# Optimization experiments

Hardware: AMD Instinct MI355X
Metric: run time of the kernel (lower is better)

Reference implementation:

```python
import jax, jax.numpy as jnp
import numpy as np

TOP_K = 2

def setup_inputs() -> dict:
    key = jax.random.key(0)
    k1, k2, k3, k4 = jax.random.split(key, 4)
    N, H, F, E = 2048, 1024, 2048, 8
    x = jax.random.normal(k1, (N, H), dtype=jnp.float32)
    router_weight = jax.random.normal(k2, (H, E), dtype=jnp.float32) * 0.02
    w1 = jax.random.normal(k3, (E, H, F), dtype=jnp.float32) * 0.02
    w2 = jax.random.normal(k4, (E, F, H), dtype=jnp.float32) * 0.02
    return {"x": x, "router_weight": router_weight, "w1": w1, "w2": w2}

def reference(x, router_weight, w1, w2):
    # Router: softmax over experts, top-k, renormalize (matches torch forward).
    N = x.shape[0]
    E = router_weight.shape[1]
    logits = x.astype(jnp.float32) @ router_weight            # [N, E]
    rprobs = jax.nn.softmax(logits, axis=-1)
    topk_p, topk_i = jax.lax.top_k(rprobs, TOP_K)             # [N, K]
    topk_p = topk_p / jnp.sum(topk_p, axis=-1, keepdims=True)
    # Scatter normalized top-k probs into dense [N, E] gate matrix; zeros
    # everywhere else, so gating subsumes the boolean routing_map.
    probs = jnp.zeros((N, E), dtype=jnp.float32).at[
        jnp.arange(N)[:, None], topk_i].set(topk_p)
    # Expert FFN (same math as permute -> grouped GEMM -> weighted scatter-add:
    # out[t] = sum_e probs[t,e] * gelu(x[t] @ w1[e]) @ w2[e]).
    h = jnp.einsum('nh,ehf->enf', x, w1)                      # [E, N, F]
    h = jax.nn.gelu(h, approximate=False)                     # torch F.gelu is erf-based
    y = jnp.einsum('enf,efh->enh', h, w2)                     # [E, N, H]
    out = jnp.einsum('enh,ne->nh', y, probs.astype(x.dtype))  # weighted combine
    return out
```

## Files before the change

### kernel.cpp

```cpp
#include <hip/hip_runtime.h>
#include <hip/hip_fp16.h>
#include <math.h>

#define NTOK 2048
#define HID  1024
#define FFN  2048
#define NEXP 8

#define BM 128
#define BN 128
#define BK 32
#define LDK 36
#define MAX_TILES 40
#define TLDA 66

#define WS_COUNTS 0
#define WS_SEG    32
#define WS_PROBS  128
#define WS_LISTS  (128 + NTOK*NEXP*4)
#define WS_XH     262144
#define WS_W2T    (WS_XH + NTOK*HID*2)
#define WS_HBUF   (WS_W2T + (size_t)NEXP*HID*FFN*2)

typedef _Float16 half8 __attribute__((ext_vector_type(8)));
typedef __fp16   fp16x2 __attribute__((ext_vector_type(2)));
typedef float    f32x4 __attribute__((ext_vector_type(4)));
typedef unsigned long long u64;

static __device__ __forceinline__ unsigned short f2h_bits(float f) {
  union { _Float16 h; unsigned short u; } v;
  v.h = (_Float16)f;
  return v.u;
}
static __device__ __forceinline__ unsigned pack2(float a, float b) {
  union { fp16x2 h; unsigned u; } v;
  v.h[0] = (__fp16)a; v.h[1] = (__fp16)b;
  return v.u;
}
static __device__ __forceinline__ unsigned cvt2(float a, float b) {
  union { fp16x2 h; unsigned u; } t;
  t.h = __builtin_amdgcn_cvt_pkrtz(a, b);
  return t.u;
}

#define GLOAD16(gsrc, ldst) \
  __builtin_amdgcn_global_load_lds( \
      (const __attribute__((address_space(1))) unsigned int*)(gsrc), \
      (__attribute__((address_space(3))) unsigned int*)(ldst), 16, 0, 0)

#define VMCNT0 asm volatile("s_waitcnt vmcnt(0)" ::: "memory")

template<int IS_W1>
static __device__ __forceinline__ void transpose4(
    int t0, const float* __restrict__ wsrc, unsigned short* __restrict__ wdst,
    unsigned short (*Ls)[64*TLDA], int tid)
{
  const int row = tid >> 2, cq = tid & 3;
  const int oc  = tid >> 2, rs = tid & 3;
  const int e = t0 >> 9;
  const int R = IS_W1 ? HID : FFN;
  const int C = IS_W1 ? FFN : HID;
  const float* src = wsrc + (size_t)e * HID * FFN;
  unsigned short* dst = wdst + (size_t)e * HID * FFN;
  float4 ld[2][4];

#define TGEOM(tt, r0v, c0v) \
    { const int rem_ = (t0 + (tt)) & 511; \
      r0v = IS_W1 ? ((rem_ >> 5) * 64) : ((rem_ >> 4) * 64); \
      c0v = IS_W1 ? ((rem_ & 31) * 64) : ((rem_ & 15) * 64); }

  {
    int r0, c0; TGEOM(0, r0, c0);
    const float4* sp = reinterpret_cast<const float4*>(
        src + (size_t)(r0 + row) * C + c0 + cq * 16);
#pragma unroll
    for (int j = 0; j < 4; ++j) ld[0][j] = sp[j];
  }
#pragma unroll
  for (int t = 0; t < 4; ++t) {
    if (t < 3) {
      int r0, c0; TGEOM(t + 1, r0, c0);
      const float4* sp = reinterpret_cast<const float4*>(
          src + (size_t)(r0 + row) * C + c0 + cq * 16);
#pragma unroll
      for (int j = 0; j < 4; ++j) ld[(t + 1) & 1][j] = sp[j];
    }
    {
      unsigned* Ld = reinterpret_cast<unsigned*>(Ls[t & 1]);
      const int dbase = row * (TLDA / 2) + cq * 8;
      const float4 a = ld[t & 1][0], b = ld[t & 1][1];
      const float4 c2 = ld[t & 1][2], d = ld[t & 1][3];
      Ld[dbase + 0] = pack2(a.x, a.y);  Ld[dbase + 1] = pack2(a.z, a.w);
      Ld[dbase + 2] = pack2(b.x, b.y);  Ld[dbase + 3] = pack2(b.z, b.w);
      Ld[dbase + 4] = pack2(c2.x, c2.y); Ld[dbase + 5] = pack2(c2.z, c2.w);
      Ld[dbase + 6] = pack2(d.x, d.y);  Ld[dbase + 7] = pack2(d.z, d.w);
    }
    __syncthreads();
    {
      int r0, c0; TGEOM(t, r0, c0);
      unsigned v[8];
#pragma unroll
      for (int j = 0; j < 8; ++j) {
        unsigned lo = Ls[t & 1][(rs * 16 + 2 * j    ) * TLDA + oc];
        unsigned hi = Ls[t & 1][(rs * 16 + 2 * j + 1) * TLDA + oc];
        v[j] = lo | (hi << 16);
      }
      unsigned short* dp = dst + (size_t)(c0 + oc) * R + r0 + rs * 16;
      *reinterpret_cast<uint4*>(dp)     = (uint4){v[0], v[1], v[2], v[3]};
      *reinterpret_cast<uint4*>(dp + 8) = (uint4){v[4], v[5], v[6], v[7]};
    }
  }
#undef TGEOM
}

__global__ __launch_bounds__(256) void moe_prep(
    const float* __restrict__ x, const float* __restrict__ rw,
    unsigned short* __restrict__ xh,
    int* __restrict__ counts, int* __restrict__ lists, float* __restrict__ probs)
{
  const int tid = threadIdx.x;
  const int wid = tid >> 6, lane = tid & 63;
  const int t = blockIdx.x * 4 + wid;

  const float* xr = x + (size_t)t * HID + lane * 16;
  const float4* xp = reinterpret_cast<const float4*>(xr);
  float4 v0 = xp[0], v1 = xp[1], v2 = xp[2], v3 = xp[3];
  float xv[16] = {v0.x,v0.y,v0.z,v0.w, v1.x,v1.y,v1.z,v1.w,
                  v2.x,v2.y,v2.z,v2.w, v3.x,v3.y,v3.z,v3.w};
  float acc[NEXP];
#pragma unroll
  for (int e = 0; e < NEXP; ++e) acc[e] = 0.f;
#pragma unroll
  for (int j = 0; j < 16; ++j) {
    const float4* rp = reinterpret_cast<const float4*>(rw + (size_t)(lane*16 + j) * NEXP);
    float4 a = rp[0], b = rp[1];
    acc[0] += xv[j]*a.x; acc[1] += xv[j]*a.y; acc[2] += xv[j]*a.z; acc[3] += xv[j]*a.w;
    acc[4] += xv[j]*b.x; acc[5] += xv[j]*b.y; acc[6] += xv[j]*b.z; acc[7] += xv[j]*b.w;
  }
#pragma unroll
  for (int off = 32; off > 0; off >>= 1) {
#pragma unroll
    for (int e = 0; e < NEXP; ++e) acc[e] += __shfl_down(acc[e], off);
  }
  unsigned short* xd = xh + (size_t)t * HID + lane * 16;
  *reinterpret_cast<uint4*>(xd) =
      (uint4){pack2(v0.x,v0.y), pack2(v0.z,v0.w), pack2(v1.x,v1.y), pack2(v1.z,v1.w)};
  *reinterpret_cast<uint4*>(xd + 8) =
      (uint4){pack2(v2.x,v2.y), pack2(v2.z,v2.w), pack2(v3.x,v3.y), pack2(v3.z,v3.w)};
  if (lane == 0) {
    float m = acc[0];
#pragma unroll
    for (int e = 1; e < NEXP; ++e) m = fmaxf(m, acc[e]);
    float p[NEXP];
#pragma unroll
    for (int e = 0; e < NEXP; ++e) p[e] = expf(acc[e] - m);
    int i0 = 0;
#pragma unroll
    for (int e = 1; e < NEXP; ++e) if (p[e] > p[i0]) i0 = e;
    int i1 = -1;
#pragma unroll
    for (int e = 0; e < NEXP; ++e) {
      if (e == i0) continue;
      if (i1 < 0 || p[e] > p[i1]) i1 = e;
    }
    const float inv = 1.f / (p[i0] + p[i1]);
    probs[t * NEXP + i0] = p[i0] * inv;
    probs[t * NEXP + i1] = p[i1] * inv;
    int pos0 = atomicAdd(&counts[i0], 1); lists[i0 * NTOK + pos0] = t;
    int pos1 = atomicAdd(&counts[i1], 1); lists[i1 * NTOK + pos1] = t;
  }
}

__global__ void moe_segoff(const int* __restrict__ counts, int* __restrict__ seg) {
  if (threadIdx.x == 0 && blockIdx.x == 0) {
    int run = 0;
    for (int e = 0; e < NEXP; ++e) {
      seg[e] = run;
      run += ((counts[e] + BM - 1) / BM) * BM;
    }
    seg[NEXP] = run;
  }
}

__global__ __launch_bounds__(256) void moe_k2(
    const unsigned short* __restrict__ xh, const float* __restrict__ w1,
    const float* __restrict__ w2, unsigned short* __restrict__ w2t,
    const int* __restrict__ counts, const int* __restrict__ seg,
    const int* __restrict__ lists, unsigned short* __restrict__ hbuf)
{
  __shared__ __align__(16) unsigned short SMEM[2*BM*BK + 2*128*LDK];
  __shared__ int tokL[BM];
  const int bid = blockIdx.x;
  const int tid = threadIdx.x;

  if (bid >= MAX_TILES * 16) {
    transpose4<0>((bid - MAX_TILES * 16) * 4, w2, w2t,
                  reinterpret_cast<unsigned short(*)[64 * TLDA]>(SMEM), tid);
    return;
  }

  const int tile = bid >> 4;
  const int jcol = bid & 15;
  const int rb = tile * BM;
  if (rb >= seg[NEXP]) return;
  int e = 0;
#pragma unroll
  for (int q = 1; q < NEXP; ++q) if (seg[q] <= rb) e = q;
  const int cnt = counts[e];
  const int rloc0 = rb - seg[e];

  unsigned short (*Asm)[BM*BK]   = reinterpret_cast<unsigned short(*)[BM*BK]>(SMEM);
  unsigned short (*Bsm)[128*LDK] = reinterpret_cast<unsigned short(*)[128*LDK]>(SMEM + 2*BM*BK);

  if (tid < BM) {
    int rl = rloc0 + tid;
    tokL[tid] = (rl < cnt) ? lists[e * NTOK + rl] : 0;
  }
  __syncthreads();

  const int lane = tid & 63;
  const int wid = tid >> 6;
  const int wr = (wid >> 1) * 64;
  const int wc = (wid & 1) * 64;
  const int lr = (lane >> 4) * 4;
  const int lc = lane & 15;
  const int khi = (lane >> 4) * 8;

  const int cw8 = (lane & 3) * 8;
  const int r0 = wid*16 + (lane >> 2);
  const unsigned short* abase[2];
  abase[0] = xh + (size_t)tokL[r0]      * HID + cw8;
  abase[1] = xh + (size_t)tokL[64 + r0] * HID + cw8;

  const int kb = tid >> 5;
  const int fb = tid & 31;
  const float* bbase = w1 + (size_t)e * HID * FFN + (size_t)jcol * 128 + fb * 4;

  f32x4 acc[4][4];
#pragma unroll
  for (int m = 0; m < 4; ++m)
#pragma unroll
    for (int n = 0; n < 4; ++n)
      acc[m][n] = (f32x4){0.f, 0.f, 0.f, 0.f};

  f32x4 bld[4];

#define LOADB1(kk) do { \
    _Pragma("unroll") \
    for (int j = 0; j < 4; ++j) \
      bld[j] = *reinterpret_cast<const f32x4*>(bbase + (size_t)((kk) + kb*4 + j) * FFN); \
  } while (0)

#define STAGEA1(buf, kk) do { \
    GLOAD16(abase[0] + (kk), &Asm[buf][(wid*64)*8]); \
    GLOAD16(abase[1] + (kk), &Asm[buf][(256 + wid*64)*8]); \
  } while (0)

#define CVTB1(buf) do { \
    _Pragma("unroll") \
    for (int i3 = 0; i3 < 4; ++i3) { \
      uint2 wv; \
      wv.x = cvt2(bld[0][i3], bld[1][i3]); \
      wv.y = cvt2(bld[2][i3], bld[3][i3]); \
      *reinterpret_cast<uint2*>(&Bsm[buf][(fb*4 + i3)*LDK + kb*4]) = wv; \
    } } while (0)

  LOADB1(0);
  STAGEA1(0, 0);
  int cur = 0;
  for (int kk = 0; kk < HID; kk += BK) {
    CVTB1(cur);
    VMCNT0;
    __syncthreads();
    if (kk + BK < HID) {
      LOADB1(kk + BK);
      STAGEA1(cur ^ 1, kk + BK);
    }
    half8 af[4], bf[4];
#pragma unroll
    for (int m = 0; m < 4; ++m)
      af[m] = *reinterpret_cast<const half8*>(&Asm[cur][(wr + m*16 + lc)*BK + khi]);
#pragma unroll
    for (int n = 0; n < 4; ++n) {
      union { u64 q[2]; half8 h; } t;
      const unsigned short* bp = &Bsm[cur][(wc + n*16 + lc)*LDK + khi];
      t.q[0] = *reinterpret_cast<const u64*>(bp);
      t.q[1] = *reinterpret_cast<const u64*>(bp + 4);
      bf[n] = t.h;
    }
#pragma unroll
    for (int m = 0; m < 4; ++m)
#pragma unroll
      for (int n = 0; n < 4; ++n)
        acc[m][n] = __builtin_amdgcn_mfma_f32_16x16x32_f16(af[m], bf[n], acc[m][n], 0, 0, 0);
    cur ^= 1;
  }
#undef LOADB1
#undef STAGEA1
#undef CVTB1

#pragma unroll
  for (int m = 0; m < 4; ++m) {
#pragma unroll
    for (int r = 0; r < 4; ++r) {
      unsigned short* hp = hbuf + (size_t)(rb + wr + m*16 + lr + r) * FFN + jcol*128 + wc + lc;
#pragma unroll
      for (int n = 0; n < 4; ++n) {
        float v = acc[m][n][r];
        float g = 0.5f * v * (1.f + erff(v * 0.70710678118f));
        hp[n*16] = f2h_bits(g);
      }
    }
  }
}

__global__ __launch_bounds__(256) void moe_gemm2(
    const unsigned short* __restrict__ hbuf, const unsigned short* __restrict__ w2t,
    const int* __restrict__ counts, const int* __restrict__ seg,
    const int* __restrict__ lists, const float* __restrict__ probs,
    float* __restrict__ out)
{
  const int tile = blockIdx.x >> 4;
  const int jcol = (blockIdx.x >> 1) & 7;
  const int ks   = blockIdx.x & 1;
  const int rb = tile * BM;
  if (rb >= seg[NEXP]) return;
  int e = 0;
#pragma unroll
  for (int q = 1; q < NEXP; ++q) if (seg[q] <= rb) e = q;
  const int cnt = counts[e];
  const int rloc0 = rb - seg[e];
  const int k0 = ks * (FFN / 2);
  const int k1 = k0 + (FFN / 2);

  __shared__ int tokL[BM];
  __shared__ float pL[BM];
  __shared__ __align__(16) unsigned short Asm[2][BM*BK];
  __shared__ __align__(16) unsigned short Bsm[2][BM*BK];

  const int tid = threadIdx.x;
  if (tid < BM) {
    int rl = rloc0 + tid;
    if (rl < cnt) {
      int tk = lists[e * NTOK + rl];
      tokL[tid] = tk;
      pL[tid] = probs[tk * NEXP + e];
    } else { tokL[tid] = 0; pL[tid] = 0.f; }
  }
  __syncthreads();

  const int lane = tid & 63;
  const int wid = tid >> 6;
  const int wr = (wid >> 1) * 64;
  const int wc = (wid & 1) * 64;
  const int lr = (lane >> 4) * 4;
  const int lc = lane & 15;
  const int khi = (lane >> 4) * 8;

  const int cw8 = (lane & 3) * 8;
  const int r0 = wid*16 + (lane >> 2);
  const unsigned short* abase[2];
  const unsigned short* bbase[2];
  abase[0] = hbuf + (size_t)(rb + r0)      * FFN + cw8;
  abase[1] = hbuf + (size_t)(rb + 64 + r0) * FFN + cw8;
  bbase[0] = w2t + ((size_t)e * HID + jcol*BN + r0)      * FFN + cw8;
  bbase[1] = w2t + ((size_t)e * HID + jcol*BN + 64 + r0) * FFN + cw8;

  f32x4 acc[4][4];
#pragma unroll
  for (int m = 0; m < 4; ++m)
#pragma unroll
    for (int n = 0; n < 4; ++n)
      acc[m][n] = (f32x4){0.f, 0.f, 0.f, 0.f};

#define STAGE2(buf, kk) do { \
    _Pragma("unroll") \
    for (int i = 0; i < 2; ++i) { \
      GLOAD16(abase[i] + (kk), &Asm[buf][(i*256 + wid*64)*8]); \
      GLOAD16(bbase[i] + (kk), &Bsm[buf][(i*256 + wid*64)*8]); \
    } } while (0)

  STAGE2(0, k0);
  VMCNT0;
  __syncthreads();
  int cur = 0;
  for (int kk = k0; kk < k1; kk += BK) {
    if (kk + BK < k1) STAGE2(cur ^ 1, kk + BK);
    half8 af[4], bf[4];
#pragma unroll
    for (int m = 0; m < 4; ++m)
      af[m] = *reinterpret_cast<const half8*>(&Asm[cur][(wr + m*16 + lc)*BK + khi]);
#pragma unroll
    for (int n = 0; n < 4; ++n)
      bf[n] = *reinterpret_cast<const half8*>(&Bsm[cur][(wc + n*16 + lc)*BK + khi]);
#pragma unroll
    for (int m = 0; m < 4; ++m)
#pragma unroll
      for (int n = 0; n < 4; ++n)
        acc[m][n] = __builtin_amdgcn_mfma_f32_16x16x32_f16(af[m], bf[n], acc[m][n], 0, 0, 0);
    VMCNT0;
    __syncthreads();
    cur ^= 1;
  }
#undef STAGE2

#pragma unroll
  for (int m = 0; m < 4; ++m) {
#pragma unroll
    for (int r = 0; r < 4; ++r) {
      const int lrow = wr + m*16 + lr + r;
      const int rl = rloc0 + lrow;
      if (rl >= cnt) continue;
      const int tok = tokL[lrow];
      const float p = pL[lrow];
      float* op = out + (size_t)tok * HID + jcol*BN + wc + lc;
#pragma unroll
      for (int n = 0; n < 4; ++n)
        atomicAdd(&op[n*16], p * acc[m][n][r]);
    }
  }
}

extern "C" void kernel_launch(void* const* d_in, const int* in_sizes, int n_in,
                              void* d_out, int out_size, void* d_ws, size_t ws_size,
                              hipStream_t stream) {
  const float* x  = (const float*)d_in[0];
  const float* rw = (const float*)d_in[1];
  const float* w1 = (const float*)d_in[2];
  const float* w2 = (const float*)d_in[3];
  float* out = (float*)d_out;

  char* ws = (char*)d_ws;
  int*   counts = (int*)(ws + WS_COUNTS);
  int*   seg    = (int*)(ws + WS_SEG);
  float* probs  = (float*)(ws + WS_PROBS);
  int*   lists  = (int*)(ws + WS_LISTS);
  unsigned short* xh   = (unsigned short*)(ws + WS_XH);
  unsigned short* w2t  = (unsigned short*)(ws + WS_W2T);
  unsigned short* hbuf = (unsigned short*)(ws + WS_HBUF);

  hipMemsetAsync(ws, 0, 128, stream);
  hipMemsetAsync(d_out, 0, (size_t)NTOK * HID * sizeof(float), stream);

  moe_prep<<<NTOK/4, 256, 0, stream>>>(x, rw, xh, counts, lists, probs);
  moe_segoff<<<1, 64, 0, stream>>>(counts, seg);
  moe_k2<<<MAX_TILES * 16 + 1024, 256, 0, stream>>>(xh, w1, w2, w2t,
                                                    counts, seg, lists, hbuf);
  moe_gemm2<<<MAX_TILES * 8 * 2, 256, 0, stream>>>(hbuf, w2t, counts, seg, lists, probs, out);
}
```

Baseline: 175.9 us.

## Fuse MoE stages into one persistent kernel with atomic work queue and dependency flags

Replaces the four separate launches (router/prep, segment offsets, GEMM1 plus W2 transpose, GEMM2) with a single persistent kernel. Blocks pull work items from an atomic counter and wait on per-stage and per-tile counters, so GEMM2 tiles can start as soon as their hidden rows are written. This removes launch gaps and the full-kernel barriers between stages. In exchange it adds spin-wait polling, extra fences and syncthreads, and relies on work items being handed out in order so a waiting block never blocks its own dependency.

```diff
diff --git a/kernel.cpp b/kernel.cpp
--- a/kernel.cpp
+++ b/kernel.cpp
@@ -8,19 +8,29 @@
 #define NEXP 8
 
 #define BM 128
-#define BN 128
 #define BK 32
 #define LDK 36
 #define MAX_TILES 40
 #define TLDA 66
 
-#define WS_COUNTS 0
-#define WS_SEG    32
-#define WS_PROBS  128
-#define WS_LISTS  (128 + NTOK*NEXP*4)
-#define WS_XH     262144
-#define WS_W2T    (WS_XH + NTOK*HID*2)
-#define WS_HBUF   (WS_W2T + (size_t)NEXP*HID*FFN*2)
+#define N_ROUTER 512
+#define N_W2T    1024
+#define N_G1     (MAX_TILES * 16)
+#define N_G2     (MAX_TILES * 8 * 2)
+#define IT_W2T   N_ROUTER
+#define IT_G1    (IT_W2T + N_W2T)
+#define IT_G2    (IT_G1 + N_G1)
+#define TOTAL_IT (IT_G2 + N_G2)
+
+#define WS_CTL    0
+#define WS_COUNTS 128
+#define WS_SEG    192
+#define WS_HROW   256
+#define WS_PROBS  512
+#define WS_LISTS  (512 + NTOK*NEXP*4)
+#define WS_XH     (WS_LISTS + NTOK*NEXP*4)
+#define WS_W2T_B  (WS_XH + (size_t)NTOK*HID*2)
+#define WS_HBUF   (WS_W2T_B + (size_t)NEXP*HID*FFN*2)
 
 typedef _Float16 half8 __attribute__((ext_vector_type(8)));
 typedef __fp16   fp16x2 __attribute__((ext_vector_type(2)));
@@ -113,149 +123,162 @@
 #undef TGEOM
 }
 
-__global__ __launch_bounds__(256) void moe_prep(
+__global__ __launch_bounds__(256) void moe_fused(
     const float* __restrict__ x, const float* __restrict__ rw,
-    unsigned short* __restrict__ xh,
-    int* __restrict__ counts, int* __restrict__ lists, float* __restrict__ probs)
-{
-  const int tid = threadIdx.x;
-  const int wid = tid >> 6, lane = tid & 63;
-  const int t = blockIdx.x * 4 + wid;
-
-  const float* xr = x + (size_t)t * HID + lane * 16;
-  const float4* xp = reinterpret_cast<const float4*>(xr);
-  float4 v0 = xp[0], v1 = xp[1], v2 = xp[2], v3 = xp[3];
-  float xv[16] = {v0.x,v0.y,v0.z,v0.w, v1.x,v1.y,v1.z,v1.w,
-                  v2.x,v2.y,v2.z,v2.w, v3.x,v3.y,v3.z,v3.w};
-  float acc[NEXP];
-#pragma unroll
-  for (int e = 0; e < NEXP; ++e) acc[e] = 0.f;
-#pragma unroll
-  for (int j = 0; j < 16; ++j) {
-    const float4* rp = reinterpret_cast<const float4*>(rw + (size_t)(lane*16 + j) * NEXP);
-    float4 a = rp[0], b = rp[1];
-    acc[0] += xv[j]*a.x; acc[1] += xv[j]*a.y; acc[2] += xv[j]*a.z; acc[3] += xv[j]*a.w;
-    acc[4] += xv[j]*b.x; acc[5] += xv[j]*b.y; acc[6] += xv[j]*b.z; acc[7] += xv[j]*b.w;
-  }
-#pragma unroll
-  for (int off = 32; off > 0; off >>= 1) {
-#pragma unroll
-    for (int e = 0; e < NEXP; ++e) acc[e] += __shfl_down(acc[e], off);
-  }
-  unsigned short* xd = xh + (size_t)t * HID + lane * 16;
-  *reinterpret_cast<uint4*>(xd) =
-      (uint4){pack2(v0.x,v0.y), pack2(v0.z,v0.w), pack2(v1.x,v1.y), pack2(v1.z,v1.w)};
-  *reinterpret_cast<uint4*>(xd + 8) =
-      (uint4){pack2(v2.x,v2.y), pack2(v2.z,v2.w), pack2(v3.x,v3.y), pack2(v3.z,v3.w)};
-  if (lane == 0) {
-    float m = acc[0];
-#pragma unroll
-    for (int e = 1; e < NEXP; ++e) m = fmaxf(m, acc[e]);
-    float p[NEXP];
-#pragma unroll
-    for (int e = 0; e < NEXP; ++e) p[e] = expf(acc[e] - m);
-    int i0 = 0;
-#pragma unroll
-    for (int e = 1; e < NEXP; ++e) if (p[e] > p[i0]) i0 = e;
-    int i1 = -1;
-#pragma unroll
-    for (int e = 0; e < NEXP; ++e) {
-      if (e == i0) continue;
-      if (i1 < 0 || p[e] > p[i1]) i1 = e;
-    }
-    const float inv = 1.f / (p[i0] + p[i1]);
-    probs[t * NEXP + i0] = p[i0] * inv;
-    probs[t * NEXP + i1] = p[i1] * inv;
-    int pos0 = atomicAdd(&counts[i0], 1); lists[i0 * NTOK + pos0] = t;
-    int pos1 = atomicAdd(&counts[i1], 1); lists[i1 * NTOK + pos1] = t;
-  }
-}
-
-__global__ void moe_segoff(const int* __restrict__ counts, int* __restrict__ seg) {
-  if (threadIdx.x == 0 && blockIdx.x == 0) {
-    int run = 0;
-    for (int e = 0; e < NEXP; ++e) {
-      seg[e] = run;
-      run += ((counts[e] + BM - 1) / BM) * BM;
-    }
-    seg[NEXP] = run;
-  }
-}
-
-__global__ __launch_bounds__(256) void moe_k2(
-    const unsigned short* __restrict__ xh, const float* __restrict__ w1,
-    const float* __restrict__ w2, unsigned short* __restrict__ w2t,
-    const int* __restrict__ counts, const int* __restrict__ seg,
-    const int* __restrict__ lists, unsigned short* __restrict__ hbuf)
+    const float* __restrict__ w1, const float* __restrict__ w2,
+    int* __restrict__ ctl, int* __restrict__ counts, int* __restrict__ seg,
+    int* __restrict__ hrow, float* __restrict__ probs, int* __restrict__ lists,
+    unsigned short* __restrict__ xh, unsigned short* __restrict__ w2t,
+    unsigned short* __restrict__ hbuf, float* __restrict__ out)
 {
   __shared__ __align__(16) unsigned short SMEM[2*BM*BK + 2*128*LDK];
   __shared__ int tokL[BM];
-  const int bid = blockIdx.x;
+  __shared__ float pL[BM];
+  __shared__ int sIt;
+
   const int tid = threadIdx.x;
-
-  if (bid >= MAX_TILES * 16) {
-    transpose4<0>((bid - MAX_TILES * 16) * 4, w2, w2t,
-                  reinterpret_cast<unsigned short(*)[64 * TLDA]>(SMEM), tid);
-    return;
-  }
-
-  const int tile = bid >> 4;
-  const int jcol = bid & 15;
-  const int rb = tile * BM;
-  if (rb >= seg[NEXP]) return;
-  int e = 0;
-#pragma unroll
-  for (int q = 1; q < NEXP; ++q) if (seg[q] <= rb) e = q;
-  const int cnt = counts[e];
-  const int rloc0 = rb - seg[e];
-
-  unsigned short (*Asm)[BM*BK]   = reinterpret_cast<unsigned short(*)[BM*BK]>(SMEM);
-  unsigned short (*Bsm)[128*LDK] = reinterpret_cast<unsigned short(*)[128*LDK]>(SMEM + 2*BM*BK);
-
-  if (tid < BM) {
-    int rl = rloc0 + tid;
-    tokL[tid] = (rl < cnt) ? lists[e * NTOK + rl] : 0;
-  }
-  __syncthreads();
-
   const int lane = tid & 63;
   const int wid = tid >> 6;
-  const int wr = (wid >> 1) * 64;
-  const int wc = (wid & 1) * 64;
-  const int lr = (lane >> 4) * 4;
-  const int lc = lane & 15;
-  const int khi = (lane >> 4) * 8;
-
-  const int cw8 = (lane & 3) * 8;
-  const int r0 = wid*16 + (lane >> 2);
-  const unsigned short* abase[2];
-  abase[0] = xh + (size_t)tokL[r0]      * HID + cw8;
-  abase[1] = xh + (size_t)tokL[64 + r0] * HID + cw8;
-
-  const int kb = tid >> 5;
-  const int fb = tid & 31;
-  const float* bbase = w1 + (size_t)e * HID * FFN + (size_t)jcol * 128 + fb * 4;
-
-  f32x4 acc[4][4];
-#pragma unroll
-  for (int m = 0; m < 4; ++m)
-#pragma unroll
-    for (int n = 0; n < 4; ++n)
-      acc[m][n] = (f32x4){0.f, 0.f, 0.f, 0.f};
-
-  f32x4 bld[4];
+  bool seen_seg = false, seen_w2t = false;
+
+  for (;;) {
+    if (tid == 0) sIt = atomicAdd(&ctl[0], 1);
+    __syncthreads();
+    const int it = sIt;
+    __syncthreads();
+    if (it >= TOTAL_IT) break;
+
+    if (it < IT_W2T) {
+      const int t = it * 4 + wid;
+      const float* xr = x + (size_t)t * HID + lane * 16;
+      const float4* xp = reinterpret_cast<const float4*>(xr);
+      float4 v0 = xp[0], v1 = xp[1], v2 = xp[2], v3 = xp[3];
+      float xv[16] = {v0.x,v0.y,v0.z,v0.w, v1.x,v1.y,v1.z,v1.w,
+                      v2.x,v2.y,v2.z,v2.w, v3.x,v3.y,v3.z,v3.w};
+      float acc[NEXP];
+#pragma unroll
+      for (int e = 0; e < NEXP; ++e) acc[e] = 0.f;
+#pragma unroll
+      for (int j = 0; j < 16; ++j) {
+        const float4* rp = reinterpret_cast<const float4*>(rw + (size_t)(lane*16 + j) * NEXP);
+        float4 a = rp[0], b = rp[1];
+        acc[0] += xv[j]*a.x; acc[1] += xv[j]*a.y; acc[2] += xv[j]*a.z; acc[3] += xv[j]*a.w;
+        acc[4] += xv[j]*b.x; acc[5] += xv[j]*b.y; acc[6] += xv[j]*b.z; acc[7] += xv[j]*b.w;
+      }
+#pragma unroll
+      for (int off = 32; off > 0; off >>= 1) {
+#pragma unroll
+        for (int e = 0; e < NEXP; ++e) acc[e] += __shfl_down(acc[e], off);
+      }
+      unsigned short* xd = xh + (size_t)t * HID + lane * 16;
+      *reinterpret_cast<uint4*>(xd) =
+          (uint4){pack2(v0.x,v0.y), pack2(v0.z,v0.w), pack2(v1.x,v1.y), pack2(v1.z,v1.w)};
+      *reinterpret_cast<uint4*>(xd + 8) =
+          (uint4){pack2(v2.x,v2.y), pack2(v2.z,v2.w), pack2(v3.x,v3.y), pack2(v3.z,v3.w)};
+      if (lane == 0) {
+        float m = acc[0];
+#pragma unroll
+        for (int e = 1; e < NEXP; ++e) m = fmaxf(m, acc[e]);
+        float p[NEXP];
+#pragma unroll
+        for (int e = 0; e < NEXP; ++e) p[e] = expf(acc[e] - m);
+        int i0 = 0;
+#pragma unroll
+        for (int e = 1; e < NEXP; ++e) if (p[e] > p[i0]) i0 = e;
+        int i1 = -1;
+#pragma unroll
+        for (int e = 0; e < NEXP; ++e) {
+          if (e == i0) continue;
+          if (i1 < 0 || p[e] > p[i1]) i1 = e;
+        }
+        const float inv = 1.f / (p[i0] + p[i1]);
+        probs[t * NEXP + i0] = p[i0] * inv;
+        probs[t * NEXP + i1] = p[i1] * inv;
+        int pos0 = atomicAdd(&counts[i0], 1); lists[i0 * NTOK + pos0] = t;
+        int pos1 = atomicAdd(&counts[i1], 1); lists[i1 * NTOK + pos1] = t;
+      }
+      __threadfence();
+      __syncthreads();
+      if (tid == 0) {
+        int old = atomicAdd(&ctl[1], 1);
+        if (old == N_ROUTER - 1) {
+          int run = 0;
+          for (int e2 = 0; e2 < NEXP; ++e2) {
+            seg[e2] = run;
+            run += ((atomicAdd(&counts[e2], 0) + BM - 1) / BM) * BM;
+          }
+          seg[NEXP] = run;
+          __threadfence();
+          atomicExch(&ctl[2], 1);
+        }
+      }
+    } else if (it < IT_G1) {
+      transpose4<0>((it - IT_W2T) * 4, w2, w2t,
+                    reinterpret_cast<unsigned short(*)[64 * TLDA]>(SMEM), tid);
+      __threadfence();
+      __syncthreads();
+      if (tid == 0) atomicAdd(&ctl[3], 1);
+    } else if (it < IT_G2) {
+      if (!seen_seg) {
+        if (tid == 0) { while (atomicAdd(&ctl[2], 0) == 0) __builtin_amdgcn_s_sleep(2); }
+        __syncthreads();
+        __threadfence();
+        seen_seg = true;
+      }
+      const int bid = it - IT_G1;
+      const int tile = bid >> 4;
+      const int jcol = bid & 15;
+      const int rb = tile * BM;
+      if (rb < seg[NEXP]) {
+        int e = 0;
+#pragma unroll
+        for (int q = 1; q < NEXP; ++q) if (seg[q] <= rb) e = q;
+        const int cnt = counts[e];
+        const int rloc0 = rb - seg[e];
+
+        unsigned short (*Asm)[BM*BK]   = reinterpret_cast<unsigned short(*)[BM*BK]>(SMEM);
+        unsigned short (*Bsm)[128*LDK] = reinterpret_cast<unsigned short(*)[128*LDK]>(SMEM + 2*BM*BK);
+
+        if (tid < BM) {
+          int rl = rloc0 + tid;
+          tokL[tid] = (rl < cnt) ? lists[e * NTOK + rl] : 0;
+        }
+        __syncthreads();
+
+        const int wr = (wid >> 1) * 64;
+        const int wc = (wid & 1) * 64;
+        const int lr = (lane >> 4) * 4;
+        const int lc = lane & 15;
+        const int khi = (lane >> 4) * 8;
+
+        const int cw8 = (lane & 3) * 8;
+        const int r0 = wid*16 + (lane >> 2);
+        const unsigned short* abase[2];
+        abase[0] = xh + (size_t)tokL[r0]      * HID + cw8;
+        abase[1] = xh + (size_t)tokL[64 + r0] * HID + cw8;
+
+        const int kb = tid >> 5;
+        const int fb = tid & 31;
+        const float* bbase = w1 + (size_t)e * HID * FFN + (size_t)jcol * 128 + fb * 4;
+
+        f32x4 acc[4][4];
+#pragma unroll
+        for (int m = 0; m < 4; ++m)
+#pragma unroll
+          for (int n = 0; n < 4; ++n)
+            acc[m][n] = (f32x4){0.f, 0.f, 0.f, 0.f};
+
+        f32x4 bld[4];
 
 #define LOADB1(kk) do { \
     _Pragma("unroll") \
     for (int j = 0; j < 4; ++j) \
       bld[j] = *reinterpret_cast<const f32x4*>(bbase + (size_t)((kk) + kb*4 + j) * FFN); \
   } while (0)
-
 #define STAGEA1(buf, kk) do { \
     GLOAD16(abase[0] + (kk), &Asm[buf][(wid*64)*8]); \
     GLOAD16(abase[1] + (kk), &Asm[buf][(256 + wid*64)*8]); \
   } while (0)
-
 #define CVTB1(buf) do { \
     _Pragma("unroll") \
     for (int i3 = 0; i3 < 4; ++i3) { \
@@ -265,113 +288,123 @@
       *reinterpret_cast<uint2*>(&Bsm[buf][(fb*4 + i3)*LDK + kb*4]) = wv; \
     } } while (0)
 
-  LOADB1(0);
-  STAGEA1(0, 0);
-  int cur = 0;
-  for (int kk = 0; kk < HID; kk += BK) {
-    CVTB1(cur);
-    VMCNT0;
-    __syncthreads();
-    if (kk + BK < HID) {
-      LOADB1(kk + BK);
-      STAGEA1(cur ^ 1, kk + BK);
-    }
-    half8 af[4], bf[4];
-#pragma unroll
-    for (int m = 0; m < 4; ++m)
-      af[m] = *reinterpret_cast<const half8*>(&Asm[cur][(wr + m*16 + lc)*BK + khi]);
-#pragma unroll
-    for (int n = 0; n < 4; ++n) {
-      union { u64 q[2]; half8 h; } t;
-      const unsigned short* bp = &Bsm[cur][(wc + n*16 + lc)*LDK + khi];
-      t.q[0] = *reinterpret_cast<const u64*>(bp);
-      t.q[1] = *reinterpret_cast<const u64*>(bp + 4);
-      bf[n] = t.h;
-    }
-#pragma unroll
-    for (int m = 0; m < 4; ++m)
-#pragma unroll
-      for (int n = 0; n < 4; ++n)
-        acc[m][n] = __builtin_amdgcn_mfma_f32_16x16x32_f16(af[m], bf[n], acc[m][n], 0, 0, 0);
-    cur ^= 1;
-  }
+        LOADB1(0);
+        STAGEA1(0, 0);
+        int cur = 0;
+        for (int kk = 0; kk < HID; kk += BK) {
+          CVTB1(cur);
+          VMCNT0;
+          __syncthreads();
+          if (kk + BK < HID) {
+            LOADB1(kk + BK);
+            STAGEA1(cur ^ 1, kk + BK);
+          }
+          half8 af[4], bf[4];
+#pragma unroll
+          for (int m = 0; m < 4; ++m)
+            af[m] = *reinterpret_cast<const half8*>(&Asm[cur][(wr + m*16 + lc)*BK + khi]);
+#pragma unroll
+          for (int n = 0; n < 4; ++n) {
+            union { u64 q[2]; half8 h; } t2;
+            const unsigned short* bp = &Bsm[cur][(wc + n*16 + lc)*LDK + khi];
+            t2.q[0] = *reinterpret_cast<const u64*>(bp);
+            t2.q[1] = *reinterpret_cast<const u64*>(bp + 4);
+            bf[n] = t2.h;
+          }
+#pragma unroll
+          for (int m = 0; m < 4; ++m)
+#pragma unroll
+            for (int n = 0; n < 4; ++n)
+              acc[m][n] = __builtin_amdgcn_mfma_f32_16x16x32_f16(af[m], bf[n], acc[m][n], 0, 0, 0);
+          __syncthreads();
+          cur ^= 1;
+        }
 #undef LOADB1
 #undef STAGEA1
 #undef CVTB1
 
 #pragma unroll
-  for (int m = 0; m < 4; ++m) {
-#pragma unroll
-    for (int r = 0; r < 4; ++r) {
-      unsigned short* hp = hbuf + (size_t)(rb + wr + m*16 + lr + r) * FFN + jcol*128 + wc + lc;
-#pragma unroll
-      for (int n = 0; n < 4; ++n) {
-        float v = acc[m][n][r];
-        float g = 0.5f * v * (1.f + erff(v * 0.70710678118f));
-        hp[n*16] = f2h_bits(g);
-      }
-    }
-  }
-}
-
-__global__ __launch_bounds__(256) void moe_gemm2(
-    const unsigned short* __restrict__ hbuf, const unsigned short* __restrict__ w2t,
-    const int* __restrict__ counts, const int* __restrict__ seg,
-    const int* __restrict__ lists, const float* __restrict__ probs,
-    float* __restrict__ out)
-{
-  const int tile = blockIdx.x >> 4;
-  const int jcol = (blockIdx.x >> 1) & 7;
-  const int ks   = blockIdx.x & 1;
-  const int rb = tile * BM;
-  if (rb >= seg[NEXP]) return;
-  int e = 0;
-#pragma unroll
-  for (int q = 1; q < NEXP; ++q) if (seg[q] <= rb) e = q;
-  const int cnt = counts[e];
-  const int rloc0 = rb - seg[e];
-  const int k0 = ks * (FFN / 2);
-  const int k1 = k0 + (FFN / 2);
-
-  __shared__ int tokL[BM];
-  __shared__ float pL[BM];
-  __shared__ __align__(16) unsigned short Asm[2][BM*BK];
-  __shared__ __align__(16) unsigned short Bsm[2][BM*BK];
-
-  const int tid = threadIdx.x;
-  if (tid < BM) {
-    int rl = rloc0 + tid;
-    if (rl < cnt) {
-      int tk = lists[e * NTOK + rl];
-      tokL[tid] = tk;
-      pL[tid] = probs[tk * NEXP + e];
-    } else { tokL[tid] = 0; pL[tid] = 0.f; }
-  }
-  __syncthreads();
-
-  const int lane = tid & 63;
-  const int wid = tid >> 6;
-  const int wr = (wid >> 1) * 64;
-  const int wc = (wid & 1) * 64;
-  const int lr = (lane >> 4) * 4;
-  const int lc = lane & 15;
-  const int khi = (lane >> 4) * 8;
-
-  const int cw8 = (lane & 3) * 8;
-  const int r0 = wid*16 + (lane >> 2);
-  const unsigned short* abase[2];
-  const unsigned short* bbase[2];
-  abase[0] = hbuf + (size_t)(rb + r0)      * FFN + cw8;
-  abase[1] = hbuf + (size_t)(rb + 64 + r0) * FFN + cw8;
-  bbase[0] = w2t + ((size_t)e * HID + jcol*BN + r0)      * FFN + cw8;
-  bbase[1] = w2t + ((size_t)e * HID + jcol*BN + 64 + r0) * FFN + cw8;
-
-  f32x4 acc[4][4];
-#pragma unroll
-  for (int m = 0; m < 4; ++m)
-#pragma unroll
-    for (int n = 0; n < 4; ++n)
-      acc[m][n] = (f32x4){0.f, 0.f, 0.f, 0.f};
+        for (int m = 0; m < 4; ++m) {
+#pragma unroll
+          for (int r = 0; r < 4; ++r) {
+            unsigned short* hp = hbuf + (size_t)(rb + wr + m*16 + lr + r) * FFN + jcol*128 + wc + lc;
+#pragma unroll
+            for (int n = 0; n < 4; ++n) {
+              float v = acc[m][n][r];
+              float g = 0.5f * v * (1.f + erff(v * 0.70710678118f));
+              hp[n*16] = f2h_bits(g);
+            }
+          }
+        }
+        __threadfence();
+        __syncthreads();
+        if (tid == 0) atomicAdd(&hrow[tile], 1);
+      }
+    } else {
+      if (!seen_seg) {
+        if (tid == 0) { while (atomicAdd(&ctl[2], 0) == 0) __builtin_amdgcn_s_sleep(2); }
+        __syncthreads();
+        __threadfence();
+        seen_seg = true;
+      }
+      if (!seen_w2t) {
+        if (tid == 0) { while (atomicAdd(&ctl[3], 0) < N_W2T) __builtin_amdgcn_s_sleep(2); }
+        __syncthreads();
+        __threadfence();
+        seen_w2t = true;
+      }
+      const int bid = it - IT_G2;
+      const int tile = bid >> 4;
+      const int jcol = (bid >> 1) & 7;
+      const int ks   = bid & 1;
+      const int rb = tile * BM;
+      if (rb < seg[NEXP]) {
+        if (tid == 0) { while (atomicAdd(&hrow[tile], 0) < 16) __builtin_amdgcn_s_sleep(2); }
+        __syncthreads();
+        __threadfence();
+
+        int e = 0;
+#pragma unroll
+        for (int q = 1; q < NEXP; ++q) if (seg[q] <= rb) e = q;
+        const int cnt = counts[e];
+        const int rloc0 = rb - seg[e];
+        const int k0 = ks * (FFN / 2);
+        const int k1 = k0 + (FFN / 2);
+
+        unsigned short (*Asm)[BM*BK] = reinterpret_cast<unsigned short(*)[BM*BK]>(SMEM);
+        unsigned short (*Bsm)[BM*BK] = reinterpret_cast<unsigned short(*)[BM*BK]>(SMEM + 2*BM*BK);
+
+        if (tid < BM) {
+          int rl = rloc0 + tid;
+          if (rl < cnt) {
+            int tk = lists[e * NTOK + rl];
+            tokL[tid] = tk;
+            pL[tid] = probs[tk * NEXP + e];
+          } else { tokL[tid] = 0; pL[tid] = 0.f; }
+        }
+        __syncthreads();
+
+        const int wr = (wid >> 1) * 64;
+        const int wc = (wid & 1) * 64;
+        const int lr = (lane >> 4) * 4;
+        const int lc = lane & 15;
+        const int khi = (lane >> 4) * 8;
+
+        const int cw8 = (lane & 3) * 8;
+        const int r0 = wid*16 + (lane >> 2);
+        const unsigned short* abase[2];
+        const unsigned short* bbase[2];
+        abase[0] = hbuf + (size_t)(rb + r0)      * FFN + cw8;
+        abase[1] = hbuf + (size_t)(rb + 64 + r0) * FFN + cw8;
+        bbase[0] = w2t + ((size_t)e * HID + jcol*128 + r0)      * FFN + cw8;
+        bbase[1] = w2t + ((size_t)e * HID + jcol*128 + 64 + r0) * FFN + cw8;
+
+        f32x4 acc[4][4];
+#pragma unroll
+        for (int m = 0; m < 4; ++m)
+#pragma unroll
+          for (int n = 0; n < 4; ++n)
+            acc[m][n] = (f32x4){0.f, 0.f, 0.f, 0.f};
 
 #define STAGE2(buf, kk) do { \
     _Pragma("unroll") \
@@ -380,43 +413,46 @@
       GLOAD16(bbase[i] + (kk), &Bsm[buf][(i*256 + wid*64)*8]); \
     } } while (0)
 
-  STAGE2(0, k0);
-  VMCNT0;
-  __syncthreads();
-  int cur = 0;
-  for (int kk = k0; kk < k1; kk += BK) {
-    if (kk + BK < k1) STAGE2(cur ^ 1, kk + BK);
-    half8 af[4], bf[4];
-#pragma unroll
-    for (int m = 0; m < 4; ++m)
-      af[m] = *reinterpret_cast<const half8*>(&Asm[cur][(wr + m*16 + lc)*BK + khi]);
-#pragma unroll
-    for (int n = 0; n < 4; ++n)
-      bf[n] = *reinterpret_cast<const half8*>(&Bsm[cur][(wc + n*16 + lc)*BK + khi]);
-#pragma unroll
-    for (int m = 0; m < 4; ++m)
-#pragma unroll
-      for (int n = 0; n < 4; ++n)
-        acc[m][n] = __builtin_amdgcn_mfma_f32_16x16x32_f16(af[m], bf[n], acc[m][n], 0, 0, 0);
-    VMCNT0;
-    __syncthreads();
-    cur ^= 1;
-  }
+        STAGE2(0, k0);
+        VMCNT0;
+        __syncthreads();
+        int cur = 0;
+        for (int kk = k0; kk < k1; kk += BK) {
+          if (kk + BK < k1) STAGE2(cur ^ 1, kk + BK);
+          half8 af[4], bf[4];
+#pragma unroll
+          for (int m = 0; m < 4; ++m)
+            af[m] = *reinterpret_cast<const half8*>(&Asm[cur][(wr + m*16 + lc)*BK + khi]);
+#pragma unroll
+          for (int n = 0; n < 4; ++n)
+            bf[n] = *reinterpret_cast<const half8*>(&Bsm[cur][(wc + n*16 + lc)*BK + khi]);
+#pragma unroll
+          for (int m = 0; m < 4; ++m)
+#pragma unroll
+            for (int n = 0; n < 4; ++n)
+              acc[m][n] = __builtin_amdgcn_mfma_f32_16x16x32_f16(af[m], bf[n], acc[m][n], 0, 0, 0);
+          VMCNT0;
+          __syncthreads();
+          cur ^= 1;
+        }
 #undef STAGE2
 
 #pragma unroll
-  for (int m = 0; m < 4; ++m) {
-#pragma unroll
-    for (int r = 0; r < 4; ++r) {
-      const int lrow = wr + m*16 + lr + r;
-      const int rl = rloc0 + lrow;
-      if (rl >= cnt) continue;
-      const int tok = tokL[lrow];
-      const float p = pL[lrow];
-      float* op = out + (size_t)tok * HID + jcol*BN + wc + lc;
-#pragma unroll
-      for (int n = 0; n < 4; ++n)
-        atomicAdd(&op[n*16], p * acc[m][n][r]);
+        for (int m = 0; m < 4; ++m) {
+#pragma unroll
+          for (int r = 0; r < 4; ++r) {
+            const int lrow = wr + m*16 + lr + r;
+            const int rl = rloc0 + lrow;
+            if (rl >= cnt) continue;
+            const int tok = tokL[lrow];
+            const float p = pL[lrow];
+            float* op = out + (size_t)tok * HID + jcol*128 + wc + lc;
+#pragma unroll
+            for (int n = 0; n < 4; ++n)
+              atomicAdd(&op[n*16], p * acc[m][n][r]);
+          }
+        }
+      }
     }
   }
 }
@@ -431,20 +467,19 @@
   float* out = (float*)d_out;
 
   char* ws = (char*)d_ws;
+  int*   ctl    = (int*)(ws + WS_CTL);
   int*   counts = (int*)(ws + WS_COUNTS);
   int*   seg    = (int*)(ws + WS_SEG);
+  int*   hrow   = (int*)(ws + WS_HROW);
   float* probs  = (float*)(ws + WS_PROBS);
   int*   lists  = (int*)(ws + WS_LISTS);
   unsigned short* xh   = (unsigned short*)(ws + WS_XH);
-  unsigned short* w2t  = (unsigned short*)(ws + WS_W2T);
+  unsigned short* w2t  = (unsigned short*)(ws + WS_W2T_B);
   unsigned short* hbuf = (unsigned short*)(ws + WS_HBUF);
 
-  hipMemsetAsync(ws, 0, 128, stream);
+  hipMemsetAsync(ws, 0, 512, stream);
   hipMemsetAsync(d_out, 0, (size_t)NTOK * HID * sizeof(float), stream);
 
-  moe_prep<<<NTOK/4, 256, 0, stream>>>(x, rw, xh, counts, lists, probs);
-  moe_segoff<<<1, 64, 0, stream>>>(counts, seg);
-  moe_k2<<<MAX_TILES * 16 + 1024, 256, 0, stream>>>(xh, w1, w2, w2t,
-                                                    counts, seg, lists, hbuf);
-  moe_gemm2<<<MAX_TILES * 8 * 2, 256, 0, stream>>>(hbuf, w2t, counts, seg, lists, probs, out);
-}
+  moe_fused<<<1024, 256, 0, stream>>>(x, rw, w1, w2, ctl, counts, seg, hrow,
+                                      probs, lists, xh, w2t, hbuf, out);
+}
```

New measurement: 566.8 us. +222.3%, slower.
